# Kernel tuning notes

Hardware: AMD Instinct MI355X
Metric: run time of the kernel (lower is better)

The kernel has to match this reference:

```python
import jax, jax.numpy as jnp
from jax import lax
import numpy as np

H = 50  # hidden size


def _lstm_layer(x, w_ih, w_hh, b_ih, b_hh):
    # x: [B, T, D_in]; returns full hidden sequence [B, T, H]
    B, T, _ = x.shape
    # precompute input contributions for all timesteps: [B, T, 4H]
    gx = jnp.einsum('bti,gi->btg', x, w_ih) + b_ih + b_hh
    gx_t = jnp.swapaxes(gx, 0, 1)  # [T, B, 4H]
    h0 = jnp.zeros((B, H), dtype=x.dtype)
    c0 = jnp.zeros((B, H), dtype=x.dtype)

    def step(carry, g_t):
        h, c = carry
        g = g_t + h @ w_hh.T  # [B, 4H]
        i, f, gg, o = jnp.split(g, 4, axis=-1)  # PyTorch gate order i,f,g,o
        i = jax.nn.sigmoid(i)
        f = jax.nn.sigmoid(f)
        gg = jnp.tanh(gg)
        o = jax.nn.sigmoid(o)
        c = f * c + i * gg
        h = o * jnp.tanh(c)
        return (h, c), h

    (_, _), hs = lax.scan(step, (h0, c0), gx_t)
    return jnp.swapaxes(hs, 0, 1)  # [B, T, H]


def setup_inputs() -> dict:
    key = jax.random.key(0)
    ks = jax.random.split(key, 12)
    s = 0.1  # weight init scale (~1/sqrt(H))
    return {
        'x': jax.random.normal(ks[0], (4096, 512, 1), dtype=jnp.float32),
        'w_ih0': jax.random.normal(ks[1], (4 * H, 1), dtype=jnp.float32) * s,
        'w_hh0': jax.random.normal(ks[2], (4 * H, H), dtype=jnp.float32) * s,
        'b_ih0': jax.random.normal(ks[3], (4 * H,), dtype=jnp.float32) * s,
        'b_hh0': jax.random.normal(ks[4], (4 * H,), dtype=jnp.float32) * s,
        'w_ih1': jax.random.normal(ks[5], (4 * H, H), dtype=jnp.float32) * s,
        'w_hh1': jax.random.normal(ks[6], (4 * H, H), dtype=jnp.float32) * s,
        'b_ih1': jax.random.normal(ks[7], (4 * H,), dtype=jnp.float32) * s,
        'b_hh1': jax.random.normal(ks[8], (4 * H,), dtype=jnp.float32) * s,
        'fc_w': jax.random.normal(ks[9], (1, H), dtype=jnp.float32) * s,
        'fc_b': jax.random.normal(ks[10], (1,), dtype=jnp.float32) * s,
    }


def reference(x, w_ih0, w_hh0, b_ih0, b_hh0, w_ih1, w_hh1, b_ih1, b_hh1, fc_w, fc_b):
    # 2-layer LSTM (dropout is identity in eval mode), last timestep -> Linear
    h1 = _lstm_layer(x, w_ih0, w_hh0, b_ih0, b_hh0)   # [B, T, H]
    h2 = _lstm_layer(h1, w_ih1, w_hh1, b_ih1, b_hh1)  # [B, T, H]
    last = h2[:, -1, :]                               # [B, H]
    return last @ fc_w.T + fc_b                       # [B, 1]
```

## Files before the change

### kernel.cpp

```cpp
#include <hip/hip_runtime.h>


#define HID 50
#define SEQ 512
#define NB 16
#define NTHREADS 1024
#define XP 516

typedef _Float16 f16x8 __attribute__((ext_vector_type(8)));
typedef float    f32x4 __attribute__((ext_vector_type(4)));

#define LOG2E 1.44269504f

__device__ __forceinline__ float lstm_cell(const f32x4 g, float& c) {
    const float ei = __builtin_amdgcn_exp2f(g[0]);
    const float ef = __builtin_amdgcn_exp2f(g[1]);
    const float eg = __builtin_amdgcn_exp2f(g[2]);
    const float eo = __builtin_amdgcn_exp2f(g[3]);
    const float A  = ei + 1.0f;
    const float F  = ef + 1.0f;
    const float G  = eg + 1.0f;
    const float AG  = A * G;
    const float den = AG * F;
    const float num = __builtin_fmaf(eg - 1.0f, F, c * AG);
    c = num * __builtin_amdgcn_rcpf(den);
    float z = c * (2.0f * LOG2E);
    z = __builtin_fminf(z, 100.0f);
    const float ec = __builtin_amdgcn_exp2f(z);
    return (ec - 1.0f) *
           __builtin_amdgcn_rcpf((eo + 1.0f) * (ec + 1.0f));
}


__global__ __launch_bounds__(NTHREADS)
void lstm2_fc_v14(const float* __restrict__ x,
                  const float* __restrict__ w_ih0,
                  const float* __restrict__ w_hh0,
                  const float* __restrict__ b_ih0,
                  const float* __restrict__ b_hh0,
                  const float* __restrict__ w_ih1,
                  const float* __restrict__ w_hh1,
                  const float* __restrict__ b_ih1,
                  const float* __restrict__ b_hh1,
                  const float* __restrict__ fc_w,
                  const float* __restrict__ fc_b,
                  float* __restrict__ out)
{
    __shared__ float xs[NB * XP];
    __shared__ f16x8 h1f[2][128];
    __shared__ f16x8 h2f[2][128];

    const int tid = threadIdx.x;
    const int b0  = blockIdx.x * NB;
    const int w   = tid >> 6;
    const int l15 = tid & 15;
    const int qq  = (tid >> 4) & 3;

    const bool dual  = (w <= 9);
    const bool hasL1 = (w <= 12);
    const bool hasL2 = dual || (w >= 13);
    const int  tL1   = w;
    const int  tL2   = dual ? w : (w - 3);

    if (dual) __builtin_amdgcn_s_setprio(1);

    for (int idx = tid; idx < NB * 128; idx += NTHREADS) {
        const int b  = idx >> 7;
        const int t4 = idx & 127;
        *(float4*)&xs[b * XP + t4 * 4] =
            *(const float4*)&x[(size_t)(b0 + b) * SEQ + t4 * 4];
    }
    if (tid < NB) {
        const float4 z = {0.f, 0.f, 0.f, 0.f};
        *(float4*)&xs[tid * XP + 512] = z;
    }
    if (tid < 256) {
        f16x8 z = {};
        h1f[tid >> 7][tid & 127] = z;
        h2f[tid >> 7][tid & 127] = z;
    }

    f16x8 wH0[2], wI1[2], wH1[2];
    {
        const int  p1  = tL1 * 16 + l15;
        const bool ok1 = hasL1 && (p1 < 4 * HID);
        const int  n1  = ok1 ? ((p1 & 3) * HID + (p1 >> 2)) : 0;
        const float s1 = ((p1 & 3) == 2) ? (2.0f * LOG2E) : -LOG2E;
        const int  p2  = tL2 * 16 + l15;
        const bool ok2 = hasL2 && (p2 < 4 * HID);
        const int  n2  = ok2 ? ((p2 & 3) * HID + (p2 >> 2)) : 0;
        const float s2 = ((p2 & 3) == 2) ? (2.0f * LOG2E) : -LOG2E;
#pragma unroll
        for (int kt = 0; kt < 2; ++kt) {
            f16x8 f0, f1, f2;
#pragma unroll
            for (int j = 0; j < 8; ++j) {
                const int k = kt * 32 + qq * 8 + j;
                float v0 = 0.0f, v1 = 0.0f, v2 = 0.0f;
                if (ok1) {
                    if (k < HID)          v0 = w_hh0[n1 * HID + k];
                    else if (k == HID)    v0 = w_ih0[n1];
                    else if (k == HID+1)  v0 = b_ih0[n1] + b_hh0[n1];
                    v0 *= s1;
                }
                if (ok2) {
                    if (k < HID)        { v1 = w_ih1[n2 * HID + k];
                                          v2 = w_hh1[n2 * HID + k]; }
                    else if (k == HID+1)  v1 = b_ih1[n2] + b_hh1[n2];
                    v1 *= s2;
                    v2 *= s2;
                }
                f0[j] = (_Float16)v0;
                f1[j] = (_Float16)v1;
                f2[j] = (_Float16)v2;
            }
            wH0[kt] = f0;
            wI1[kt] = f1;
            wH1[kt] = f2;
        }
    }

    const int juL1   = tL1 * 4 + qq;
    const int juL2   = tL2 * 4 + qq;
    const int wOffL1 = ((((juL1 >> 5) * 4) + ((juL1 >> 3) & 3)) * 16 + l15) * 8 + (juL1 & 7);
    const int wOffL2 = ((((juL2 >> 5) * 4) + ((juL2 >> 3) & 3)) * 16 + l15) * 8 + (juL2 & 7);
    const int rdo = qq * 16 + l15;
    const float* xrow = xs + l15 * XP;
    const f32x4 z4 = {0.f, 0.f, 0.f, 0.f};

    float c1 = 0.f, c2 = 0.f;

    __syncthreads();

    if (tid < NB) {
        _Float16* e0 = (_Float16*)&h1f[0][96 + tid];
        e0[2] = (_Float16)xs[tid * XP];
        e0[3] = (_Float16)1.0f;
        ((_Float16*)&h1f[1][96 + tid])[3] = (_Float16)1.0f;
    }
    __syncthreads();

    auto phase = [&](const f16x8* __restrict__ h1o, const f16x8* __restrict__ h2o,
                     f16x8* __restrict__ h1n, f16x8* __restrict__ h2n,
                     int p, bool doL1, bool doL2) {
        const f16x8 hb0 = h1o[rdo];
        const f16x8 hb1 = h1o[64 + rdo];
        if (hasL2 && doL2) {
            const f16x8 sb0 = h2o[rdo];
            const f16x8 sb1 = h2o[64 + rdo];
            f32x4 acc_a, acc_b;
            acc_a = __builtin_amdgcn_mfma_f32_16x16x32_f16(wI1[0], hb0, z4,    0, 0, 0);
            acc_a = __builtin_amdgcn_mfma_f32_16x16x32_f16(wI1[1], hb1, acc_a, 0, 0, 0);
            acc_b = __builtin_amdgcn_mfma_f32_16x16x32_f16(wH1[0], sb0, z4,    0, 0, 0);
            acc_b = __builtin_amdgcn_mfma_f32_16x16x32_f16(wH1[1], sb1, acc_b, 0, 0, 0);
            const f32x4 acc = acc_a + acc_b;
            ((_Float16*)h2n)[wOffL2] = (_Float16)lstm_cell(acc, c2);
        }
        if (hasL1 && doL1) {
            f32x4 acc;
            acc = __builtin_amdgcn_mfma_f32_16x16x32_f16(wH0[0], hb0, z4,  0, 0, 0);
            acc = __builtin_amdgcn_mfma_f32_16x16x32_f16(wH0[1], hb1, acc, 0, 0, 0);
            const _Float16 hw = (_Float16)lstm_cell(acc, c1);
            if (w < 12) {
                ((_Float16*)h1n)[wOffL1] = hw;
            } else {
                if (qq < 2)       ((_Float16*)h1n)[wOffL1] = hw;
                else if (qq == 2) ((_Float16*)h1n)[wOffL1] =
                                      (_Float16)xrow[p + 1];
            }
        }
        __syncthreads();
    };

    phase(h1f[0], h2f[0], h1f[1], h2f[1], 0, true, false);
#pragma unroll 1
    for (int p = 1; p <= 509; p += 2) {
        phase(h1f[1], h2f[1], h1f[0], h2f[0], p,     true, true);
        phase(h1f[0], h2f[0], h1f[1], h2f[1], p + 1, true, true);
    }
    phase(h1f[1], h2f[1], h1f[0], h2f[0], 511, true,  true);
    phase(h1f[0], h2f[0], h1f[1], h2f[1], 512, false, true);

    if (tid < NB) {
        const int m = tid;
        const _Float16* h2e = (const _Float16*)h2f[1];
        float s = fc_b[0];
        for (int j = 0; j < HID; ++j) {
            const int chunk = (((j >> 5) * 4) + ((j >> 3) & 3)) * 16 + m;
            s += fc_w[j] * (float)h2e[chunk * 8 + (j & 7)];
        }
        out[b0 + m] = s;
    }
}

extern "C" void kernel_launch(void* const* d_in, const int* in_sizes, int n_in,
                              void* d_out, int out_size, void* d_ws, size_t ws_size,
                              hipStream_t stream) {
    const float* x     = (const float*)d_in[0];
    const float* w_ih0 = (const float*)d_in[1];
    const float* w_hh0 = (const float*)d_in[2];
    const float* b_ih0 = (const float*)d_in[3];
    const float* b_hh0 = (const float*)d_in[4];
    const float* w_ih1 = (const float*)d_in[5];
    const float* w_hh1 = (const float*)d_in[6];
    const float* b_ih1 = (const float*)d_in[7];
    const float* b_hh1 = (const float*)d_in[8];
    const float* fc_w  = (const float*)d_in[9];
    const float* fc_b  = (const float*)d_in[10];
    float* out = (float*)d_out;

    const int B = in_sizes[0] / SEQ;

    lstm2_fc_v14<<<B / NB, NTHREADS, 0, stream>>>(
        x, w_ih0, w_hh0, b_ih0, b_hh0, w_ih1, w_hh1, b_ih1, b_hh1, fc_w, fc_b, out);
}
```

Measured before the change: 390.9 us.

## Halve block size and give each wave two gate tiles per layer

Cuts the block from 16 to 8 waves. Each wave now owns up to two 16-row gate tiles for layer 1 and/or layer 2, and keeps two cell states per layer in registers. The goal is cheaper per-timestep __syncthreads barriers, and possibly more blocks resident per CU. The cost is a longer serial chain of MFMAs and cell math per wave each step, plus higher register pressure from the doubled weight fragments.

```diff
diff --git a/kernel.cpp b/kernel.cpp
--- a/kernel.cpp
+++ b/kernel.cpp
@@ -4,7 +4,7 @@
 #define HID 50
 #define SEQ 512
 #define NB 16
-#define NTHREADS 1024
+#define NTHREADS 512
 #define XP 516
 
 typedef _Float16 f16x8 __attribute__((ext_vector_type(8)));
@@ -33,7 +33,7 @@
 
 
 __global__ __launch_bounds__(NTHREADS)
-void lstm2_fc_v14(const float* __restrict__ x,
+void lstm2_fc_v16(const float* __restrict__ x,
                   const float* __restrict__ w_ih0,
                   const float* __restrict__ w_hh0,
                   const float* __restrict__ b_ih0,
@@ -56,13 +56,15 @@
     const int l15 = tid & 15;
     const int qq  = (tid >> 4) & 3;
 
-    const bool dual  = (w <= 9);
-    const bool hasL1 = (w <= 12);
-    const bool hasL2 = dual || (w >= 13);
-    const int  tL1   = w;
-    const int  tL2   = dual ? w : (w - 3);
-
-    if (dual) __builtin_amdgcn_s_setprio(1);
+    const int nL1 = (w <= 4) ? 2 : 1;
+    const int nL2 = (w <= 1 || w >= 5) ? 2 : 1;
+    int tL1[2], tL2[2];
+    tL1[0] = (w <= 4) ? 2 * w     : (w + 5);
+    tL1[1] = (w <= 4) ? 2 * w + 1 : -1;
+    tL2[0] = (w <= 1) ? 2 * w     : ((w <= 4) ? (w + 2) : (2 * w - 3));
+    tL2[1] = (w <= 1) ? 2 * w + 1 : ((w >= 5) ? (2 * w - 2) : -1);
+
+    if (w <= 1) __builtin_amdgcn_s_setprio(1);
 
     for (int idx = tid; idx < NB * 128; idx += NTHREADS) {
         const int b  = idx >> 7;
@@ -80,14 +82,15 @@
         h2f[tid >> 7][tid & 127] = z;
     }
 
-    f16x8 wH0[2], wI1[2], wH1[2];
-    {
-        const int  p1  = tL1 * 16 + l15;
-        const bool ok1 = hasL1 && (p1 < 4 * HID);
+    f16x8 wH0[2][2], wI1[2][2], wH1[2][2];
+#pragma unroll
+    for (int s = 0; s < 2; ++s) {
+        const int  p1  = tL1[s] * 16 + l15;
+        const bool ok1 = (s < nL1) && (tL1[s] >= 0) && (p1 < 4 * HID);
         const int  n1  = ok1 ? ((p1 & 3) * HID + (p1 >> 2)) : 0;
         const float s1 = ((p1 & 3) == 2) ? (2.0f * LOG2E) : -LOG2E;
-        const int  p2  = tL2 * 16 + l15;
-        const bool ok2 = hasL2 && (p2 < 4 * HID);
+        const int  p2  = tL2[s] * 16 + l15;
+        const bool ok2 = (s < nL2) && (tL2[s] >= 0) && (p2 < 4 * HID);
         const int  n2  = ok2 ? ((p2 & 3) * HID + (p2 >> 2)) : 0;
         const float s2 = ((p2 & 3) == 2) ? (2.0f * LOG2E) : -LOG2E;
 #pragma unroll
@@ -114,21 +117,27 @@
                 f1[j] = (_Float16)v1;
                 f2[j] = (_Float16)v2;
             }
-            wH0[kt] = f0;
-            wI1[kt] = f1;
-            wH1[kt] = f2;
-        }
-    }
-
-    const int juL1   = tL1 * 4 + qq;
-    const int juL2   = tL2 * 4 + qq;
-    const int wOffL1 = ((((juL1 >> 5) * 4) + ((juL1 >> 3) & 3)) * 16 + l15) * 8 + (juL1 & 7);
-    const int wOffL2 = ((((juL2 >> 5) * 4) + ((juL2 >> 3) & 3)) * 16 + l15) * 8 + (juL2 & 7);
+            wH0[s][kt] = f0;
+            wI1[s][kt] = f1;
+            wH1[s][kt] = f2;
+        }
+    }
+
+    int  wOffL1[2], wOffL2[2];
+    bool isXT[2];
+#pragma unroll
+    for (int s = 0; s < 2; ++s) {
+        const int ju1 = tL1[s] * 4 + qq;
+        wOffL1[s] = ((((ju1 >> 5) * 4) + ((ju1 >> 3) & 3)) * 16 + l15) * 8 + (ju1 & 7);
+        const int ju2 = tL2[s] * 4 + qq;
+        wOffL2[s] = ((((ju2 >> 5) * 4) + ((ju2 >> 3) & 3)) * 16 + l15) * 8 + (ju2 & 7);
+        isXT[s] = (tL1[s] == 12);
+    }
     const int rdo = qq * 16 + l15;
     const float* xrow = xs + l15 * XP;
     const f32x4 z4 = {0.f, 0.f, 0.f, 0.f};
 
-    float c1 = 0.f, c2 = 0.f;
+    float c1[2] = {0.f, 0.f}, c2[2] = {0.f, 0.f};
 
     __syncthreads();
 
@@ -145,28 +154,34 @@
                      int p, bool doL1, bool doL2) {
         const f16x8 hb0 = h1o[rdo];
         const f16x8 hb1 = h1o[64 + rdo];
-        if (hasL2 && doL2) {
+        if (doL2) {
             const f16x8 sb0 = h2o[rdo];
             const f16x8 sb1 = h2o[64 + rdo];
-            f32x4 acc_a, acc_b;
-            acc_a = __builtin_amdgcn_mfma_f32_16x16x32_f16(wI1[0], hb0, z4,    0, 0, 0);
-            acc_a = __builtin_amdgcn_mfma_f32_16x16x32_f16(wI1[1], hb1, acc_a, 0, 0, 0);
-            acc_b = __builtin_amdgcn_mfma_f32_16x16x32_f16(wH1[0], sb0, z4,    0, 0, 0);
-            acc_b = __builtin_amdgcn_mfma_f32_16x16x32_f16(wH1[1], sb1, acc_b, 0, 0, 0);
-            const f32x4 acc = acc_a + acc_b;
-            ((_Float16*)h2n)[wOffL2] = (_Float16)lstm_cell(acc, c2);
-        }
-        if (hasL1 && doL1) {
-            f32x4 acc;
-            acc = __builtin_amdgcn_mfma_f32_16x16x32_f16(wH0[0], hb0, z4,  0, 0, 0);
-            acc = __builtin_amdgcn_mfma_f32_16x16x32_f16(wH0[1], hb1, acc, 0, 0, 0);
-            const _Float16 hw = (_Float16)lstm_cell(acc, c1);
-            if (w < 12) {
-                ((_Float16*)h1n)[wOffL1] = hw;
-            } else {
-                if (qq < 2)       ((_Float16*)h1n)[wOffL1] = hw;
-                else if (qq == 2) ((_Float16*)h1n)[wOffL1] =
-                                      (_Float16)xrow[p + 1];
+#pragma unroll
+            for (int s = 0; s < 2; ++s) if (s < nL2) {
+                f32x4 acc_a, acc_b;
+                acc_a = __builtin_amdgcn_mfma_f32_16x16x32_f16(wI1[s][0], hb0, z4,    0, 0, 0);
+                acc_a = __builtin_amdgcn_mfma_f32_16x16x32_f16(wI1[s][1], hb1, acc_a, 0, 0, 0);
+                acc_b = __builtin_amdgcn_mfma_f32_16x16x32_f16(wH1[s][0], sb0, z4,    0, 0, 0);
+                acc_b = __builtin_amdgcn_mfma_f32_16x16x32_f16(wH1[s][1], sb1, acc_b, 0, 0, 0);
+                const f32x4 acc = acc_a + acc_b;
+                ((_Float16*)h2n)[wOffL2[s]] = (_Float16)lstm_cell(acc, c2[s]);
+            }
+        }
+        if (doL1) {
+#pragma unroll
+            for (int s = 0; s < 2; ++s) if (s < nL1) {
+                f32x4 acc;
+                acc = __builtin_amdgcn_mfma_f32_16x16x32_f16(wH0[s][0], hb0, z4,  0, 0, 0);
+                acc = __builtin_amdgcn_mfma_f32_16x16x32_f16(wH0[s][1], hb1, acc, 0, 0, 0);
+                const _Float16 hw = (_Float16)lstm_cell(acc, c1[s]);
+                if (!isXT[s]) {
+                    ((_Float16*)h1n)[wOffL1[s]] = hw;
+                } else {
+                    if (qq < 2)       ((_Float16*)h1n)[wOffL1[s]] = hw;
+                    else if (qq == 2) ((_Float16*)h1n)[wOffL1[s]] =
+                                          (_Float16)xrow[p + 1];
+                }
             }
         }
         __syncthreads();
@@ -211,6 +226,6 @@
 
     const int B = in_sizes[0] / SEQ;
 
-    lstm2_fc_v14<<<B / NB, NTHREADS, 0, stream>>>(
+    lstm2_fc_v16<<<B / NB, NTHREADS, 0, stream>>>(
         x, w_ih0, w_hh0, b_ih0, b_hh0, w_ih1, w_hh1, b_ih1, b_hh1, fc_w, fc_b, out);
 }
```

After: 436.6 us. 1.12x slower.
